# Kernel optimization log

Measured on AMD Instinct MI355X. Metric: run time of the kernel, lower is better.

The kernel has to match this reference:

```python
import jax, jax.numpy as jnp
import numpy as np

LN_EPS = 1e-5

def layer_norm(x, w, b):
    mu = jnp.mean(x, axis=-1, keepdims=True)
    var = jnp.var(x, axis=-1, keepdims=True)
    return (x - mu) * jax.lax.rsqrt(var + LN_EPS) * w + b

def masked_softmax_topk(ctx, k):
    # ctx: [B, D, D]; keep top-k per row (scatter-style mask), softmax over last dim
    B, D, _ = ctx.shape
    idx = jax.lax.top_k(ctx, k)[1]                       # [B, D, k]
    mask = jnp.zeros(ctx.shape, bool).at[
        jnp.arange(B)[:, None, None], jnp.arange(D)[None, :, None], idx
    ].set(True)
    return jax.nn.softmax(jnp.where(mask, ctx, -jnp.inf), axis=-1)

def setup_inputs() -> dict:
    key = jax.random.key(0)
    ks = jax.random.split(key, 8)
    B, H, W, C = 8, 96, 96, 256
    x1 = jax.random.normal(ks[0], (B, H, W, C), jnp.float32)
    x2 = jax.random.normal(ks[1], (B, H, W, C), jnp.float32)
    norm1_w = jnp.ones((C,), jnp.float32)
    norm1_b = jnp.zeros((C,), jnp.float32)
    reproj_w = jax.random.normal(ks[2], (2 * C, C), jnp.float32) * (1.0 / np.sqrt(C))  # 1x1 conv
    reproj_b = jnp.zeros((2 * C,), jnp.float32)
    norm2_w = jnp.ones((2 * C,), jnp.float32)
    norm2_b = jnp.zeros((2 * C,), jnp.float32)
    attn_w = jnp.full((4,), 0.25, jnp.float32)  # attn1..attn4 scalars
    return {"x1": x1, "x2": x2, "norm1_w": norm1_w, "norm1_b": norm1_b,
            "reproj_w": reproj_w, "reproj_b": reproj_b,
            "norm2_w": norm2_w, "norm2_b": norm2_b, "attn_w": attn_w}

def reference(x1, x2, norm1_w, norm1_b, reproj_w, reproj_b, norm2_w, norm2_b, attn_w):
    B, H, W, C = x1.shape
    N, D = H * W, C  # head_count = 1
    n1 = layer_norm(x1.reshape(B, N, C), norm1_w, norm1_b)   # values source
    n2 = layer_norm(x2.reshape(B, N, C), norm1_w, norm1_b)   # keys/queries source
    kq = jnp.swapaxes(n2, 1, 2)                              # [B, D, N]
    values = jnp.swapaxes(n1, 1, 2)                          # [B, D, N]
    keyv = jax.nn.softmax(kq, axis=2)                        # softmax over N
    query = jax.nn.softmax(kq, axis=1)                       # softmax over channels
    context = jnp.einsum('bdn,ben->bde', keyv, values)       # [B, D, D]
    ks = [D // 2, (D * 2) // 3, (D * 3) // 4, (D * 4) // 5]
    attended = jnp.zeros((B, D, N), x1.dtype)
    for i, k in enumerate(ks):
        attn = masked_softmax_topk(context, k)               # [B, D, D]
        attended = attended + attn_w[i] * jnp.einsum('bde,ben->bdn', attn, query)
    # 1x1 conv reprojection D -> 2D, then LayerNorm over 2D
    rp = jnp.einsum('od,bdn->bno', reproj_w, attended) + reproj_b  # [B, N, 2D]
    rp = layer_norm(rp, norm2_w, norm2_b)
    out = rp.reshape(B, H, W, 2 * C).transpose(0, 3, 1, 2)   # [B, 2C, H, W]
    return out
```

## Files before the change

### kernel.cpp

```cpp
#include <hip/hip_runtime.h>
#include <math.h>

typedef __attribute__((ext_vector_type(8))) short short8;
typedef __attribute__((ext_vector_type(4))) float f32x4;
typedef unsigned short u16;

constexpr int Bb = 8;
constexpr int Nn = 9216;
constexpr int Cc = 256;
constexpr int Oo = 512;
constexpr float LN_EPS = 1e-5f;
constexpr int KS2 = 16;

static __device__ __forceinline__ u16 f2bf(float f) {
    unsigned u = __builtin_bit_cast(unsigned, f);
    u += 0x7fffu + ((u >> 16) & 1u);
    return (u16)(u >> 16);
}
static __device__ __forceinline__ float bf2f(u16 u) {
    return __builtin_bit_cast(float, (unsigned)u << 16);
}

__global__ __launch_bounds__(512, 2) void k_pre(const float* __restrict__ src,
                                                const float* __restrict__ lnw,
                                                const float* __restrict__ lnb,
                                                u16* __restrict__ dstT,
                                                u16* __restrict__ Qexp,
                                                float* __restrict__ pS,
                                                int doExp) {
    __shared__ u16 tile[256][72];
    __shared__ float wsh[256], bsh[256];
    const int b = blockIdx.z, nc = blockIdx.x;
    const int n0 = nc * 64;
    const int t = threadIdx.x;
    if (t < 256) { wsh[t] = lnw[t]; bsh[t] = lnb[t]; }
    __syncthreads();

    const int r = t >> 3;
    const int g = t & 7;
    const long long row = (long long)b * Nn + n0 + r;
    const float* rowp = src + row * Cc;

    float4 v[8];
#pragma unroll
    for (int i = 0; i < 8; ++i)
        v[i] = *reinterpret_cast<const float4*>(rowp + g * 4 + i * 32);

    float s = 0.f, q = 0.f;
#pragma unroll
    for (int i = 0; i < 8; ++i) {
        s += v[i].x + v[i].y + v[i].z + v[i].w;
        q += v[i].x * v[i].x + v[i].y * v[i].y + v[i].z * v[i].z + v[i].w * v[i].w;
    }
    s += __shfl_xor(s, 1); s += __shfl_xor(s, 2); s += __shfl_xor(s, 4);
    q += __shfl_xor(q, 1); q += __shfl_xor(q, 2); q += __shfl_xor(q, 4);
    const float mu = s * (1.0f / Cc);
    const float rstd = rsqrtf(q * (1.0f / Cc) - mu * mu + LN_EPS);

    float se = 0.f;
#pragma unroll
    for (int i = 0; i < 8; ++i) {
        const int d = g * 4 + i * 32;
        const float4 w4 = *reinterpret_cast<const float4*>(&wsh[d]);
        const float4 b4 = *reinterpret_cast<const float4*>(&bsh[d]);
        v[i].x = (v[i].x - mu) * rstd * w4.x + b4.x;
        v[i].y = (v[i].y - mu) * rstd * w4.y + b4.y;
        v[i].z = (v[i].z - mu) * rstd * w4.z + b4.z;
        v[i].w = (v[i].w - mu) * rstd * w4.w + b4.w;
        if (doExp) {
            v[i].x = __expf(v[i].x); v[i].y = __expf(v[i].y);
            v[i].z = __expf(v[i].z); v[i].w = __expf(v[i].w);
            se += v[i].x + v[i].y + v[i].z + v[i].w;
        }
        tile[d + 0][r] = f2bf(v[i].x);
        tile[d + 1][r] = f2bf(v[i].y);
        tile[d + 2][r] = f2bf(v[i].z);
        tile[d + 3][r] = f2bf(v[i].w);
    }

    if (doExp) {
        se += __shfl_xor(se, 1); se += __shfl_xor(se, 2); se += __shfl_xor(se, 4);
        const float inv = 1.0f / se;
#pragma unroll
        for (int i = 0; i < 8; ++i) {
            const int d = g * 4 + i * 32;
            int2 pk;
            pk.x = (int)((unsigned)f2bf(v[i].x * inv) | ((unsigned)f2bf(v[i].y * inv) << 16));
            pk.y = (int)((unsigned)f2bf(v[i].z * inv) | ((unsigned)f2bf(v[i].w * inv) << 16));
            *reinterpret_cast<int2*>(Qexp + row * Cc + d) = pk;
        }
    }
    __syncthreads();

#pragma unroll
    for (int p = 0; p < 4; ++p) {
        const int d = p * 64 + (t >> 3);
        const int c = (t & 7) * 8;
        const int4 u = *reinterpret_cast<const int4*>(&tile[d][c]);
        *reinterpret_cast<int4*>(dstT + ((long long)(b * Cc + d)) * Nn + n0 + c) = u;
        if (doExp) {
            const unsigned uu[4] = {(unsigned)u.x, (unsigned)u.y, (unsigned)u.z, (unsigned)u.w};
            float ss = 0.f;
#pragma unroll
            for (int j = 0; j < 4; ++j) {
                ss += bf2f((u16)(uu[j] & 0xffff));
                ss += bf2f((u16)(uu[j] >> 16));
            }
            ss += __shfl_xor(ss, 1);
            ss += __shfl_xor(ss, 2);
            ss += __shfl_xor(ss, 4);
            if ((t & 7) == 0) pS[((long long)b * 144 + nc) * Cc + d] = ss;
        }
    }
}

__global__ __launch_bounds__(256) void k_colcomb(const float* __restrict__ pS,
                                                 float* __restrict__ colS) {
    const int d = threadIdx.x, b = blockIdx.x;
    float s = 0.f;
    for (int c = 0; c < 144; ++c) s += pS[((long long)b * 144 + c) * Cc + d];
    colS[b * Cc + d] = s;
}

__global__ __launch_bounds__(256) void k_mm_bf16(const u16* __restrict__ A,
                                                 const u16* __restrict__ Bt,
                                                 float* __restrict__ C,
                                                 int lda, int ldb, int ldc,
                                                 long long sAb, long long sBb, long long sCb,
                                                 int kChunk, long long sCk,
                                                 int tilesN, int kIters) {
    __shared__ alignas(16) u16 Asm[128 * 64];
    __shared__ alignas(16) u16 Bsm[128 * 64];
    const int t = threadIdx.x;
    const int b = blockIdx.z, kc = blockIdx.y;
    const int tm = blockIdx.x / tilesN, tn = blockIdx.x % tilesN;
    const int m0 = tm * 128, n0 = tn * 128;
    const u16* Ag = A + b * sAb + (long long)kc * kChunk;
    const u16* Bg = Bt + b * sBb + (long long)kc * kChunk;
    float* Cg = C + b * sCb + (long long)kc * sCk;

    const int l = t & 63, w = t >> 6;
    const int wr = w >> 1, wc = w & 1;
    const int frow = l & 15, fk = (l >> 4) << 3;

    f32x4 acc[4][4] = {};

    for (int kt = 0; kt < kIters; ++kt) {
        const int k0 = kt * 64;
        int4 av[4], bv[4];
#pragma unroll
        for (int i = 0; i < 4; ++i) {
            const int s = t + 256 * i;
            const int r = s >> 3, c16 = s & 7;
            av[i] = *reinterpret_cast<const int4*>(Ag + (long long)(m0 + r) * lda + k0 + c16 * 8);
            bv[i] = *reinterpret_cast<const int4*>(Bg + (long long)(n0 + r) * ldb + k0 + c16 * 8);
        }
        __syncthreads();
#pragma unroll
        for (int i = 0; i < 4; ++i) {
            const int s = t + 256 * i;
            const int r = s >> 3, c16 = s & 7;
            const int idx = r * 64 + ((c16 * 8) ^ ((r & 7) << 3));
            *reinterpret_cast<int4*>(&Asm[idx]) = av[i];
            *reinterpret_cast<int4*>(&Bsm[idx]) = bv[i];
        }
        __syncthreads();
#pragma unroll
        for (int kf = 0; kf < 2; ++kf) {
            short8 af[4], bf[4];
            const int kk = kf * 32 + fk;
#pragma unroll
            for (int mi = 0; mi < 4; ++mi) {
                const int row = wr * 64 + mi * 16 + frow;
                af[mi] = *reinterpret_cast<const short8*>(&Asm[row * 64 + (kk ^ ((row & 7) << 3))]);
            }
#pragma unroll
            for (int ni = 0; ni < 4; ++ni) {
                const int row = wc * 64 + ni * 16 + frow;
                bf[ni] = *reinterpret_cast<const short8*>(&Bsm[row * 64 + (kk ^ ((row & 7) << 3))]);
            }
#pragma unroll
            for (int mi = 0; mi < 4; ++mi)
#pragma unroll
                for (int ni = 0; ni < 4; ++ni)
                    acc[mi][ni] = __builtin_amdgcn_mfma_f32_16x16x32_bf16(af[mi], bf[ni], acc[mi][ni], 0, 0, 0);
        }
    }

    const int crow0 = (l >> 4) * 4, ccol = l & 15;
#pragma unroll
    for (int mi = 0; mi < 4; ++mi) {
#pragma unroll
        for (int ni = 0; ni < 4; ++ni) {
            const int row = m0 + wr * 64 + mi * 16 + crow0;
            const int col = n0 + wc * 64 + ni * 16 + ccol;
#pragma unroll
            for (int r_ = 0; r_ < 4; ++r_)
                Cg[(long long)(row + r_) * ldc + col] = acc[mi][ni][r_];
        }
    }
}

__global__ __launch_bounds__(256) void k_ctxred(const float* __restrict__ ctxp,
                                                const float* __restrict__ colS,
                                                float* __restrict__ ctx) {
    const long long i4 = ((long long)blockIdx.x * 256 + threadIdx.x) * 4;
    float4 s = make_float4(0.f, 0.f, 0.f, 0.f);
    for (int kc = 0; kc < KS2; ++kc) {
        const float4 v = *reinterpret_cast<const float4*>(ctxp + (long long)kc * (Bb * Cc * Cc) + i4);
        s.x += v.x; s.y += v.y; s.z += v.z; s.w += v.w;
    }
    const int b = (int)(i4 >> 16);
    const int d = ((int)(i4 >> 8)) & 255;
    const float inv = 1.0f / colS[b * Cc + d];
    s.x *= inv; s.y *= inv; s.z *= inv; s.w *= inv;
    *reinterpret_cast<float4*>(ctx + i4) = s;
}

__global__ __launch_bounds__(256) void k_rank(const float* __restrict__ ctx,
                                              const float* __restrict__ aw,
                                              float* __restrict__ Ac) {
    __shared__ float row[256];
    __shared__ float red[256];
    const int d = blockIdx.x, b = blockIdx.y, e = threadIdx.x;
    const float c = ctx[((long long)(b * Cc + d)) * Cc + e];
    row[e] = c;
    __syncthreads();
    int p = 0;
    for (int j = 0; j < 256; ++j) {
        const float cj = row[j];
        p += (cj > c) || (cj == c && j < e);
    }
    red[e] = c; __syncthreads();
    for (int s_ = 128; s_; s_ >>= 1) { if (e < s_) red[e] = fmaxf(red[e], red[e + s_]); __syncthreads(); }
    const float m = red[0];
    const float ex = __expf(c - m);
    const int kks[4] = {128, 170, 192, 204};
    float Zv[4];
#pragma unroll
    for (int i = 0; i < 4; ++i) {
        __syncthreads();
        red[e] = (p < kks[i]) ? ex : 0.0f;
        __syncthreads();
        for (int s_ = 128; s_; s_ >>= 1) { if (e < s_) red[e] += red[e + s_]; __syncthreads(); }
        Zv[i] = red[0];
    }
    float wsum = 0.0f;
#pragma unroll
    for (int i = 0; i < 4; ++i)
        if (p < kks[i]) wsum += aw[i] / Zv[i];
    Ac[((long long)(b * Cc + d)) * Cc + e] = ex * wsum;
}

__global__ __launch_bounds__(256) void k_wa(const float* __restrict__ W,
                                            const float* __restrict__ Ac,
                                            u16* __restrict__ WAb16) {
    __shared__ float As[16][64], Bs[16][64];
    const int b = blockIdx.y;
    const int o0 = (blockIdx.x >> 2) * 64, e0 = (blockIdx.x & 3) * 64;
    const int t = threadIdx.x, tx = t & 15, ty = t >> 4;
    const int a_oo = t >> 2, a_k4 = (t & 3) * 4;
    const int b_kk = t >> 4, b_e4 = (t & 15) * 4;
    float acc[4][4] = {{0.f}};
    for (int kd = 0; kd < 256; kd += 16) {
        const float4 wv = *reinterpret_cast<const float4*>(W + (o0 + a_oo) * Cc + kd + a_k4);
        const float4 av = *reinterpret_cast<const float4*>(Ac + ((long long)(b * Cc + kd + b_kk)) * Cc + e0 + b_e4);
        __syncthreads();
        As[a_k4 + 0][a_oo] = wv.x; As[a_k4 + 1][a_oo] = wv.y;
        As[a_k4 + 2][a_oo] = wv.z; As[a_k4 + 3][a_oo] = wv.w;
        *reinterpret_cast<float4*>(&Bs[b_kk][b_e4]) = av;
        __syncthreads();
#pragma unroll
        for (int kk = 0; kk < 16; ++kk) {
            const float4 a4 = *reinterpret_cast<const float4*>(&As[kk][ty * 4]);
            const float4 b4 = *reinterpret_cast<const float4*>(&Bs[kk][tx * 4]);
            const float aa[4] = {a4.x, a4.y, a4.z, a4.w};
            const float bb[4] = {b4.x, b4.y, b4.z, b4.w};
#pragma unroll
            for (int i = 0; i < 4; ++i)
#pragma unroll
                for (int j = 0; j < 4; ++j) acc[i][j] = fmaf(aa[i], bb[j], acc[i][j]);
        }
    }
#pragma unroll
    for (int i = 0; i < 4; ++i) {
        int2 pk;
        pk.x = (int)((unsigned)f2bf(acc[i][0]) | ((unsigned)f2bf(acc[i][1]) << 16));
        pk.y = (int)((unsigned)f2bf(acc[i][2]) | ((unsigned)f2bf(acc[i][3]) << 16));
        *reinterpret_cast<int2*>(WAb16 + ((long long)(b * Oo + o0 + ty * 4 + i)) * Cc + e0 + tx * 4) = pk;
    }
}

__global__ __launch_bounds__(256, 3) void k_rpln(const u16* __restrict__ Qexp,
                                                 const u16* __restrict__ WAb16,
                                                 const float* __restrict__ rbias,
                                                 const float* __restrict__ nw,
                                                 const float* __restrict__ nb,
                                                 float* __restrict__ out) {
    __shared__ float patch[4][16][36];
    __shared__ float psum[32][4], psq[32][4];
    __shared__ float muA[32], rsA[32];

    const int t = threadIdx.x;
    const int b = blockIdx.z;
    const int n0 = blockIdx.x * 32;
    const int l = t & 63, w = t >> 6;
    const int frow = l & 15, fk = (l >> 4) << 3;
    const int hi = l >> 4;

    f32x4 acc[2][8] = {};

    const u16* Aq = Qexp + ((long long)b * Nn + n0) * Cc;
    const u16* Bw = WAb16 + ((long long)b * Oo + w * 128) * Cc;

    int4 aF[2][8];
#pragma unroll
    for (int mi = 0; mi < 2; ++mi)
#pragma unroll
        for (int s = 0; s < 8; ++s)
            aF[mi][s] = *reinterpret_cast<const int4*>(Aq + (mi * 16 + frow) * Cc + s * 32 + fk);

    int4 bC[8], bN[8];
#pragma unroll
    for (int ni = 0; ni < 8; ++ni)
        bC[ni] = *reinterpret_cast<const int4*>(Bw + (ni * 16 + frow) * Cc + fk);

#pragma unroll
    for (int s = 0; s < 8; ++s) {
        if (s < 7) {
            const int kk = (s + 1) * 32 + fk;
#pragma unroll
            for (int ni = 0; ni < 8; ++ni)
                bN[ni] = *reinterpret_cast<const int4*>(Bw + (ni * 16 + frow) * Cc + kk);
        }
#pragma unroll
        for (int mi = 0; mi < 2; ++mi)
#pragma unroll
            for (int ni = 0; ni < 8; ++ni)
                acc[mi][ni] = __builtin_amdgcn_mfma_f32_16x16x32_bf16(
                    __builtin_bit_cast(short8, aF[mi][s]), __builtin_bit_cast(short8, bC[ni]),
                    acc[mi][ni], 0, 0, 0);
        if (s < 7) {
#pragma unroll
            for (int ni = 0; ni < 8; ++ni) bC[ni] = bN[ni];
        }
    }

#pragma unroll
    for (int ni = 0; ni < 8; ++ni) {
        const float bb = rbias[w * 128 + ni * 16 + frow];
#pragma unroll
        for (int mi = 0; mi < 2; ++mi)
#pragma unroll
            for (int r_ = 0; r_ < 4; ++r_) acc[mi][ni][r_] += bb;
    }
#pragma unroll
    for (int mi = 0; mi < 2; ++mi)
#pragma unroll
        for (int r_ = 0; r_ < 4; ++r_) {
            float s = 0.f, q = 0.f;
#pragma unroll
            for (int ni = 0; ni < 8; ++ni) { const float v = acc[mi][ni][r_]; s += v; q += v * v; }
#pragma unroll
            for (int m = 8; m; m >>= 1) { s += __shfl_xor(s, m); q += __shfl_xor(q, m); }
            if (frow == 0) {
                const int row = mi * 16 + hi * 4 + r_;
                psum[row][w] = s; psq[row][w] = q;
            }
        }
    __syncthreads();
    if (t < 32) {
        const float s = psum[t][0] + psum[t][1] + psum[t][2] + psum[t][3];
        const float q = psq[t][0] + psq[t][1] + psq[t][2] + psq[t][3];
        const float m = s * (1.0f / Oo);
        muA[t] = m;
        rsA[t] = rsqrtf(q * (1.0f / Oo) - m * m + LN_EPS);
    }
    __syncthreads();

    float nwv[8], nbv[8];
#pragma unroll
    for (int ni = 0; ni < 8; ++ni) {
        const int o = w * 128 + ni * 16 + frow;
        nwv[ni] = nw[o]; nbv[ni] = nb[o];
    }

#pragma unroll
    for (int ni = 0; ni < 8; ++ni) {
#pragma unroll
        for (int mi = 0; mi < 2; ++mi)
#pragma unroll
            for (int r_ = 0; r_ < 4; ++r_) {
                const int nl = mi * 16 + hi * 4 + r_;
                patch[w][frow][nl] = (acc[mi][ni][r_] - muA[nl]) * rsA[nl] * nwv[ni] + nbv[ni];
            }
        asm volatile("s_waitcnt lgkmcnt(0)" ::: "memory");
        __builtin_amdgcn_sched_barrier(0);
#pragma unroll
        for (int p = 0; p < 2; ++p) {
            const int o_loc = p * 8 + (l >> 3);
            const int colf4 = l & 7;
            const float4 v = *reinterpret_cast<const float4*>(&patch[w][o_loc][colf4 * 4]);
            const int o_g = w * 128 + ni * 16 + o_loc;
            *reinterpret_cast<float4*>(&out[((long long)(b * Oo + o_g)) * Nn + n0 + colf4 * 4]) = v;
        }
        asm volatile("s_waitcnt lgkmcnt(0)" ::: "memory");
        __builtin_amdgcn_sched_barrier(0);
    }
}

extern "C" void kernel_launch(void* const* d_in, const int* in_sizes, int n_in,
                              void* d_out, int out_size, void* d_ws, size_t ws_size,
                              hipStream_t stream) {
    (void)in_sizes; (void)n_in; (void)out_size; (void)ws_size;
    const float* x1    = (const float*)d_in[0];
    const float* x2    = (const float*)d_in[1];
    const float* n1w   = (const float*)d_in[2];
    const float* n1b   = (const float*)d_in[3];
    const float* rw    = (const float*)d_in[4];
    const float* rbias = (const float*)d_in[5];
    const float* n2w   = (const float*)d_in[6];
    const float* n2b   = (const float*)d_in[7];
    const float* aw    = (const float*)d_in[8];
    float* out = (float*)d_out;

    u16* KexpT = (u16*)d_out;
    u16* VT    = KexpT + (size_t)Bb * Nn * Cc;

    float* ws = (float*)d_ws;
    size_t off = 0;
    u16*   Qexp   = (u16*)(ws + off); off += (size_t)Bb * Nn * Cc / 2;
    float* ctxp   = ws + off; off += (size_t)KS2 * Bb * Cc * Cc;
    float* ctx    = ws + off; off += (size_t)Bb * Cc * Cc;
    float* Ac     = ws + off; off += (size_t)Bb * Cc * Cc;
    u16*   WAb16  = (u16*)(ws + off); off += (size_t)Bb * Oo * Cc / 2;
    float* pS     = ws + off; off += (size_t)Bb * 144 * Cc;
    float* colS   = ws + off; off += (size_t)Bb * Cc;

    k_pre<<<dim3(144, 1, Bb), 512, 0, stream>>>(x2, n1w, n1b, KexpT, Qexp, pS, 1);
    k_pre<<<dim3(144, 1, Bb), 512, 0, stream>>>(x1, n1w, n1b, VT, Qexp, pS, 0);
    k_colcomb<<<dim3(Bb), 256, 0, stream>>>(pS, colS);
    k_mm_bf16<<<dim3(4, KS2, Bb), 256, 0, stream>>>(
        KexpT, VT, ctxp,
        Nn, Nn, Cc,
        (long long)Cc * Nn, (long long)Cc * Nn, (long long)Cc * Cc,
        Nn / KS2, (long long)Bb * Cc * Cc,
        Cc / 128, (Nn / KS2) / 64);
    k_ctxred<<<dim3(512), 256, 0, stream>>>(ctxp, colS, ctx);
    k_rank<<<dim3(Cc, Bb), 256, 0, stream>>>(ctx, aw, Ac);
    k_wa<<<dim3(32, Bb), 256, 0, stream>>>(rw, Ac, WAb16);
    k_rpln<<<dim3(288, 1, Bb), 256, 0, stream>>>(Qexp, WAb16, rbias, n2w, n2b, out);
}
```

Before: 272.5 us.

## Stage reprojection GEMM tiles through swizzled LDS with 64-row blocks

```diff
diff --git a/kernel.cpp b/kernel.cpp
--- a/kernel.cpp
+++ b/kernel.cpp
@@ -291,64 +291,82 @@
     }
 }
 
-__global__ __launch_bounds__(256, 3) void k_rpln(const u16* __restrict__ Qexp,
+__global__ __launch_bounds__(512, 2) void k_rpln(const u16* __restrict__ Qexp,
                                                  const u16* __restrict__ WAb16,
                                                  const float* __restrict__ rbias,
                                                  const float* __restrict__ nw,
                                                  const float* __restrict__ nb,
                                                  float* __restrict__ out) {
-    __shared__ float patch[4][16][36];
-    __shared__ float psum[32][4], psq[32][4];
-    __shared__ float muA[32], rsA[32];
+    __shared__ alignas(16) unsigned char smemRaw[73728];
+    __shared__ float psum[64][4], psq[64][4];
+    __shared__ float muA[64], rsA[64];
+
+    u16* Ab = reinterpret_cast<u16*>(smemRaw);
+    u16* Bbuf = reinterpret_cast<u16*>(smemRaw + 8192);
+    float (*patch)[16][36] = reinterpret_cast<float (*)[16][36]>(smemRaw);
 
     const int t = threadIdx.x;
     const int b = blockIdx.z;
-    const int n0 = blockIdx.x * 32;
+    const int n0 = blockIdx.x * 64;
     const int l = t & 63, w = t >> 6;
-    const int frow = l & 15, fk = (l >> 4) << 3;
-    const int hi = l >> 4;
+    const int wr = w >> 2, wc = w & 3;
+    const int frow = l & 15, hi = l >> 4;
+
+    const u16* Ag = Qexp + ((long long)b * Nn + n0) * Cc;
+    const u16* Bg = WAb16 + (long long)b * Oo * Cc;
+
+    const int sr = t >> 3;
+    const int skb = t & 7;
 
     f32x4 acc[2][8] = {};
 
-    const u16* Aq = Qexp + ((long long)b * Nn + n0) * Cc;
-    const u16* Bw = WAb16 + ((long long)b * Oo + w * 128) * Cc;
-
-    int4 aF[2][8];
-#pragma unroll
-    for (int mi = 0; mi < 2; ++mi)
-#pragma unroll
-        for (int s = 0; s < 8; ++s)
-            aF[mi][s] = *reinterpret_cast<const int4*>(Aq + (mi * 16 + frow) * Cc + s * 32 + fk);
-
-    int4 bC[8], bN[8];
-#pragma unroll
-    for (int ni = 0; ni < 8; ++ni)
-        bC[ni] = *reinterpret_cast<const int4*>(Bw + (ni * 16 + frow) * Cc + fk);
-
-#pragma unroll
-    for (int s = 0; s < 8; ++s) {
-        if (s < 7) {
-            const int kk = (s + 1) * 32 + fk;
-#pragma unroll
-            for (int ni = 0; ni < 8; ++ni)
-                bN[ni] = *reinterpret_cast<const int4*>(Bw + (ni * 16 + frow) * Cc + kk);
-        }
-#pragma unroll
-        for (int mi = 0; mi < 2; ++mi)
-#pragma unroll
-            for (int ni = 0; ni < 8; ++ni)
-                acc[mi][ni] = __builtin_amdgcn_mfma_f32_16x16x32_bf16(
-                    __builtin_bit_cast(short8, aF[mi][s]), __builtin_bit_cast(short8, bC[ni]),
-                    acc[mi][ni], 0, 0, 0);
-        if (s < 7) {
-#pragma unroll
-            for (int ni = 0; ni < 8; ++ni) bC[ni] = bN[ni];
+    int4 aR, bR[8];
+    aR = *reinterpret_cast<const int4*>(Ag + (long long)sr * Cc + skb * 8);
+#pragma unroll
+    for (int i = 0; i < 8; ++i)
+        bR[i] = *reinterpret_cast<const int4*>(Bg + (long long)(i * 64 + sr) * Cc + skb * 8);
+
+    for (int kt = 0; kt < 4; ++kt) {
+        if (kt) __syncthreads();
+        *reinterpret_cast<int4*>(&Ab[sr * 64 + ((skb ^ (sr & 7)) * 8)]) = aR;
+#pragma unroll
+        for (int i = 0; i < 8; ++i) {
+            const int rB = i * 64 + sr;
+            *reinterpret_cast<int4*>(&Bbuf[rB * 64 + ((skb ^ (rB & 7)) * 8)]) = bR[i];
+        }
+        __syncthreads();
+        if (kt < 3) {
+            const int k0 = (kt + 1) * 64;
+            aR = *reinterpret_cast<const int4*>(Ag + (long long)sr * Cc + k0 + skb * 8);
+#pragma unroll
+            for (int i = 0; i < 8; ++i)
+                bR[i] = *reinterpret_cast<const int4*>(Bg + (long long)(i * 64 + sr) * Cc + k0 + skb * 8);
+        }
+#pragma unroll
+        for (int kf = 0; kf < 2; ++kf) {
+            const int j = kf * 4 + hi;
+            short8 af[2], bf[8];
+#pragma unroll
+            for (int mi = 0; mi < 2; ++mi) {
+                const int row = wr * 32 + mi * 16 + frow;
+                af[mi] = *reinterpret_cast<const short8*>(&Ab[row * 64 + ((j ^ (row & 7)) * 8)]);
+            }
+#pragma unroll
+            for (int ni = 0; ni < 8; ++ni) {
+                const int row = wc * 128 + ni * 16 + frow;
+                bf[ni] = *reinterpret_cast<const short8*>(&Bbuf[row * 64 + ((j ^ (row & 7)) * 8)]);
+            }
+#pragma unroll
+            for (int mi = 0; mi < 2; ++mi)
+#pragma unroll
+                for (int ni = 0; ni < 8; ++ni)
+                    acc[mi][ni] = __builtin_amdgcn_mfma_f32_16x16x32_bf16(af[mi], bf[ni], acc[mi][ni], 0, 0, 0);
         }
     }
 
 #pragma unroll
     for (int ni = 0; ni < 8; ++ni) {
-        const float bb = rbias[w * 128 + ni * 16 + frow];
+        const float bb = rbias[wc * 128 + ni * 16 + frow];
 #pragma unroll
         for (int mi = 0; mi < 2; ++mi)
 #pragma unroll
@@ -364,12 +382,12 @@
 #pragma unroll
             for (int m = 8; m; m >>= 1) { s += __shfl_xor(s, m); q += __shfl_xor(q, m); }
             if (frow == 0) {
-                const int row = mi * 16 + hi * 4 + r_;
-                psum[row][w] = s; psq[row][w] = q;
+                const int row = wr * 32 + mi * 16 + hi * 4 + r_;
+                psum[row][wc] = s; psq[row][wc] = q;
             }
         }
     __syncthreads();
-    if (t < 32) {
+    if (t < 64) {
         const float s = psum[t][0] + psum[t][1] + psum[t][2] + psum[t][3];
         const float q = psq[t][0] + psq[t][1] + psq[t][2] + psq[t][3];
         const float m = s * (1.0f / Oo);
@@ -381,7 +399,7 @@
     float nwv[8], nbv[8];
 #pragma unroll
     for (int ni = 0; ni < 8; ++ni) {
-        const int o = w * 128 + ni * 16 + frow;
+        const int o = wc * 128 + ni * 16 + frow;
         nwv[ni] = nw[o]; nbv[ni] = nb[o];
     }
 
@@ -392,7 +410,8 @@
 #pragma unroll
             for (int r_ = 0; r_ < 4; ++r_) {
                 const int nl = mi * 16 + hi * 4 + r_;
-                patch[w][frow][nl] = (acc[mi][ni][r_] - muA[nl]) * rsA[nl] * nwv[ni] + nbv[ni];
+                const int row = wr * 32 + nl;
+                patch[w][frow][nl] = (acc[mi][ni][r_] - muA[row]) * rsA[row] * nwv[ni] + nbv[ni];
             }
         asm volatile("s_waitcnt lgkmcnt(0)" ::: "memory");
         __builtin_amdgcn_sched_barrier(0);
@@ -401,8 +420,8 @@
             const int o_loc = p * 8 + (l >> 3);
             const int colf4 = l & 7;
             const float4 v = *reinterpret_cast<const float4*>(&patch[w][o_loc][colf4 * 4]);
-            const int o_g = w * 128 + ni * 16 + o_loc;
-            *reinterpret_cast<float4*>(&out[((long long)(b * Oo + o_g)) * Nn + n0 + colf4 * 4]) = v;
+            const int o_g = wc * 128 + ni * 16 + o_loc;
+            *reinterpret_cast<float4*>(&out[((long long)(b * Oo + o_g)) * Nn + n0 + wr * 32 + colf4 * 4]) = v;
         }
         asm volatile("s_waitcnt lgkmcnt(0)" ::: "memory");
         __builtin_amdgcn_sched_barrier(0);
@@ -449,5 +468,5 @@
     k_ctxred<<<dim3(512), 256, 0, stream>>>(ctxp, colS, ctx);
     k_rank<<<dim3(Cc, Bb), 256, 0, stream>>>(ctx, aw, Ac);
     k_wa<<<dim3(32, Bb), 256, 0, stream>>>(rw, Ac, WAb16);
-    k_rpln<<<dim3(288, 1, Bb), 256, 0, stream>>>(Qexp, WAb16, rbias, n2w, n2b, out);
-}
+    k_rpln<<<dim3(144, 1, Bb), 512, 0, stream>>>(Qexp, WAb16, rbias, n2w, n2b, out);
+}
```

Result: slower. 300.3 us (+10.2%).

## Stage reprojection GEMM operands through LDS via direct global-to-LDS loads

Applied to the files above, without the earlier changes.

```diff
diff --git a/kernel.cpp b/kernel.cpp
--- a/kernel.cpp
+++ b/kernel.cpp
@@ -19,6 +19,13 @@
 }
 static __device__ __forceinline__ float bf2f(u16 u) {
     return __builtin_bit_cast(float, (unsigned)u << 16);
+}
+
+static __device__ __forceinline__ void gl_lds16(const u16* g, u16* l) {
+    __builtin_amdgcn_global_load_lds(
+        (const __attribute__((address_space(1))) void*)g,
+        (__attribute__((address_space(3))) void*)l,
+        16, 0, 0);
 }
 
 __global__ __launch_bounds__(512, 2) void k_pre(const float* __restrict__ src,
@@ -291,59 +298,63 @@
     }
 }
 
-__global__ __launch_bounds__(256, 3) void k_rpln(const u16* __restrict__ Qexp,
+__global__ __launch_bounds__(256, 4) void k_rpln(const u16* __restrict__ Qexp,
                                                  const u16* __restrict__ WAb16,
                                                  const float* __restrict__ rbias,
                                                  const float* __restrict__ nw,
                                                  const float* __restrict__ nb,
                                                  float* __restrict__ out) {
-    __shared__ float patch[4][16][36];
+    __shared__ alignas(16) unsigned char smemRaw[34816];
     __shared__ float psum[32][4], psq[32][4];
     __shared__ float muA[32], rsA[32];
+
+    u16* Ab   = reinterpret_cast<u16*>(smemRaw);
+    u16* Bbuf = reinterpret_cast<u16*>(smemRaw + 2048);
+    float (*patch)[16][36] = reinterpret_cast<float (*)[16][36]>(smemRaw);
 
     const int t = threadIdx.x;
     const int b = blockIdx.z;
     const int n0 = blockIdx.x * 32;
     const int l = t & 63, w = t >> 6;
-    const int frow = l & 15, fk = (l >> 4) << 3;
-    const int hi = l >> 4;
+    const int frow = l & 15, hi = l >> 4;
+
+    const u16* Aq = Qexp + ((long long)b * Nn + n0) * Cc;
+    const u16* Bg = WAb16 + ((long long)b * Oo) * Cc;
 
     f32x4 acc[2][8] = {};
 
-    const u16* Aq = Qexp + ((long long)b * Nn + n0) * Cc;
-    const u16* Bw = WAb16 + ((long long)b * Oo + w * 128) * Cc;
-
-    int4 aF[2][8];
-#pragma unroll
-    for (int mi = 0; mi < 2; ++mi)
-#pragma unroll
-        for (int s = 0; s < 8; ++s)
-            aF[mi][s] = *reinterpret_cast<const int4*>(Aq + (mi * 16 + frow) * Cc + s * 32 + fk);
-
-    int4 bC[8], bN[8];
-#pragma unroll
-    for (int ni = 0; ni < 8; ++ni)
-        bC[ni] = *reinterpret_cast<const int4*>(Bw + (ni * 16 + frow) * Cc + fk);
-
-#pragma unroll
-    for (int s = 0; s < 8; ++s) {
-        if (s < 7) {
-            const int kk = (s + 1) * 32 + fk;
+    for (int kt = 0; kt < 8; ++kt) {
+        const int k0 = kt * 32;
+        if (kt) __syncthreads();
+#pragma unroll
+        for (int i = 0; i < 8; ++i) {
+            const int r = i * 64 + (t >> 2);
+            const int c = (t & 3) ^ ((r >> 1) & 3);
+            gl_lds16(Bg + (long long)r * Cc + k0 + c * 8, Bbuf + i * 2048 + t * 8);
+        }
+        if (t < 128) {
+            const int r = t >> 2;
+            const int c = (t & 3) ^ ((r >> 1) & 3);
+            gl_lds16(Aq + (long long)r * Cc + k0 + c * 8, Ab + t * 8);
+        }
+        __syncthreads();
+
+        short8 af[2], bf[8];
+#pragma unroll
+        for (int mi = 0; mi < 2; ++mi) {
+            const int row = mi * 16 + frow;
+            af[mi] = *reinterpret_cast<const short8*>(&Ab[row * 32 + ((hi ^ ((row >> 1) & 3)) * 8)]);
+        }
+#pragma unroll
+        for (int ni = 0; ni < 8; ++ni) {
+            const int row = w * 128 + ni * 16 + frow;
+            bf[ni] = *reinterpret_cast<const short8*>(&Bbuf[row * 32 + ((hi ^ ((row >> 1) & 3)) * 8)]);
+        }
+#pragma unroll
+        for (int mi = 0; mi < 2; ++mi)
 #pragma unroll
             for (int ni = 0; ni < 8; ++ni)
-                bN[ni] = *reinterpret_cast<const int4*>(Bw + (ni * 16 + frow) * Cc + kk);
-        }
-#pragma unroll
-        for (int mi = 0; mi < 2; ++mi)
-#pragma unroll
-            for (int ni = 0; ni < 8; ++ni)
-                acc[mi][ni] = __builtin_amdgcn_mfma_f32_16x16x32_bf16(
-                    __builtin_bit_cast(short8, aF[mi][s]), __builtin_bit_cast(short8, bC[ni]),
-                    acc[mi][ni], 0, 0, 0);
-        if (s < 7) {
-#pragma unroll
-            for (int ni = 0; ni < 8; ++ni) bC[ni] = bN[ni];
-        }
+                acc[mi][ni] = __builtin_amdgcn_mfma_f32_16x16x32_bf16(af[mi], bf[ni], acc[mi][ni], 0, 0, 0);
     }
 
 #pragma unroll
```

New measurement: 284.8 us. 1.04x slower.
